# Kernel optimization log

Measured on AMD Instinct MI355X. Metric: run time of the kernel, lower is better.

The kernel has to match this reference:

```python
import jax, jax.numpy as jnp
import numpy as np

NUM_HEADS = 16
INACTIVE = 4          # cfg_comp.attention_heads_inactive
SIG_DIM = 64          # cfg_comp.attention_heads_signature_dim
MLP_HIDDEN = 512      # cfg_comp.attention_heads_inference_mlp_hidden


def setup_inputs() -> dict:
    key = jax.random.key(0)
    ks = jax.random.split(key, 16)
    S, B, E = 2048, 2, 1024
    def xavier(k, shape, gain=1.0):
        fan_in, fan_out = shape[1], shape[0]
        a = gain * np.sqrt(6.0 / (fan_in + fan_out))
        return jax.random.uniform(k, shape, jnp.float32, -a, a)
    g = 1.0 / np.sqrt(2.0)
    return {
        "query": jax.random.normal(ks[0], (S, B, E), jnp.float32),
        "q_w": xavier(ks[1], (E, E), g), "q_b": jnp.zeros((E,), jnp.float32),
        "k_w": xavier(ks[2], (E, E), g), "k_b": jnp.zeros((E,), jnp.float32),
        "v_w": xavier(ks[3], (E, E), g), "v_b": jnp.zeros((E,), jnp.float32),
        "out_w": xavier(ks[4], (E, E)), "out_b": jnp.zeros((E,), jnp.float32),
        "inf1_w": xavier(ks[5], (MLP_HIDDEN, E), np.sqrt(2.0)),
        "inf1_b": jnp.zeros((MLP_HIDDEN,), jnp.float32),
        "inf2_w": xavier(ks[6], (SIG_DIM, MLP_HIDDEN), np.sqrt(2.0)),
        "inf2_b": jnp.zeros((SIG_DIM,), jnp.float32),
        "head_sig": jax.random.normal(ks[7], (NUM_HEADS, SIG_DIM), jnp.float32)
                    * np.sqrt(2.0 / (NUM_HEADS + SIG_DIM)),
    }


def _head_mask(query, inf1_w, inf1_b, inf2_w, inf2_b, head_sig):
    # inference_masking_step: (S, B, E) -> binary mask (B, H, S)
    t = jax.nn.relu(query @ inf1_w.T + inf1_b)          # (S, B, hidden)
    t = t @ inf2_w.T + inf2_b                            # (S, B, sig)
    s = t @ head_sig.T                                   # (S, B, H) head scores
    keep = NUM_HEADS - INACTIVE
    kth = jax.lax.top_k(s, keep)[0][..., -1]             # (S, B) kth-largest score
    mask = (s >= kth[..., None]).astype(query.dtype)     # 1 at top-`keep` heads
    mask = jax.lax.stop_gradient(mask)                   # scatter of constants in torch
    return jnp.transpose(mask, (1, 2, 0))                # (B, H, S)


def reference(query, q_w, q_b, k_w, k_b, v_w, v_b, out_w, out_b,
              inf1_w, inf1_b, inf2_w, inf2_b, head_sig):
    S, B, E = query.shape
    H, D = NUM_HEADS, E // NUM_HEADS
    scaling = D ** (-0.5)

    q = (query @ q_w.T + q_b) * scaling                  # (S, B, E)
    k = query @ k_w.T + k_b
    v = query @ v_w.T + v_b
    # (S, B, E) -> (B, H, S, D)
    to_bhsd = lambda x: jnp.transpose(x.reshape(S, B, H, D), (1, 2, 0, 3))
    q, k, v = to_bhsd(q), to_bhsd(k), to_bhsd(v)

    attn = jax.nn.softmax(jnp.einsum("bhqd,bhkd->bhqk", q, k), axis=-1)
    o = jnp.einsum("bhqk,bhkd->bhqd", attn, v)           # (B, H, S, D)

    mask = _head_mask(query, inf1_w, inf1_b, inf2_w, inf2_b, head_sig)  # (B, H, S)
    o = o * mask[..., None]                              # gate per head per position

    out = jnp.transpose(o, (2, 0, 1, 3)).reshape(S, B, E)
    return out @ out_w.T + out_b
```

## Files before the change

kernel.cpp:

```cpp
#include <hip/hip_runtime.h>
#include <hip/hip_bf16.h>

#define S_LEN 2048
#define BATCH 2
#define EDIM 1024
#define NHEAD 16
#define DHEAD 64
#define HIDDEN 512
#define SIGD 64
#define KEEP 12

typedef __attribute__((ext_vector_type(8))) short bf16x8;
typedef __attribute__((ext_vector_type(4))) float f32x4;

static __device__ __forceinline__ float bf2f(short s) {
  unsigned int u = ((unsigned int)(unsigned short)s) << 16;
  float f; __builtin_memcpy(&f, &u, 4); return f;
}
static __device__ __forceinline__ short f2bf(float f) {
  unsigned int u; __builtin_memcpy(&u, &f, 4);
  u += 0x7fffu + ((u >> 16) & 1u);
  return (short)(u >> 16);
}

#if __has_builtin(__builtin_amdgcn_exp2f)
static __device__ __forceinline__ float fexp2(float x) { return __builtin_amdgcn_exp2f(x); }
#else
static __device__ __forceinline__ float fexp2(float x) { return exp2f(x); }
#endif

static __device__ __forceinline__ void gl_lds16(const short* g, short* l) {
  __builtin_amdgcn_global_load_lds(
      (const __attribute__((address_space(1))) unsigned int*)g,
      (__attribute__((address_space(3))) unsigned int*)l, 16, 0, 0);
}

template<int CTRL>
static __device__ __forceinline__ float dpp_movf(float x) {
  return __builtin_bit_cast(float, __builtin_amdgcn_update_dpp(
      0, __builtin_bit_cast(int, x), CTRL, 0xF, 0xF, true));
}
static __device__ __forceinline__ float row_max16(float v) {
  v = fmaxf(v, dpp_movf<0x128>(v));
  v = fmaxf(v, dpp_movf<0x124>(v));
  v = fmaxf(v, dpp_movf<0x122>(v));
  v = fmaxf(v, dpp_movf<0x121>(v));
  return v;
}
static __device__ __forceinline__ float row_sum16(float v) {
  v += dpp_movf<0x128>(v);
  v += dpp_movf<0x124>(v);
  v += dpp_movf<0x122>(v);
  v += dpp_movf<0x121>(v);
  return v;
}

__global__ __launch_bounds__(256) void cvt_all(
    const float* __restrict__ query, const float* __restrict__ inf1_w,
    const float* __restrict__ qw, const float* __restrict__ kw,
    const float* __restrict__ vw, const float* __restrict__ ow,
    short* __restrict__ qh, short* __restrict__ ql,
    short* __restrict__ w1h, short* __restrict__ w1l,
    short* __restrict__ Wq, short* __restrict__ Wk,
    short* __restrict__ Wv, short* __restrict__ Wo)
{
  int blk = blockIdx.x;
  if (blk < 4608) {
    const float* in; short *oh, *ol; int i;
    if (blk < 4096) { in = query;  oh = qh;  ol = ql;  i = (blk * 256 + threadIdx.x) * 4; }
    else            { in = inf1_w; oh = w1h; ol = w1l; i = ((blk - 4096) * 256 + threadIdx.x) * 4; }
    float4 f = *(const float4*)(in + i);
    union { short s[4]; uint2 v; } uh, ul;
    float x[4] = {f.x, f.y, f.z, f.w};
    #pragma unroll
    for (int u = 0; u < 4; ++u) {
      short h = f2bf(x[u]);
      uh.s[u] = h;
      ul.s[u] = f2bf(x[u] - bf2f(h));
    }
    *(uint2*)(oh + i) = uh.v;
    *(uint2*)(ol + i) = ul.v;
  } else {
    int t = blk - 4608;
    int mat = t >> 10, sub = t & 1023;
    const float* in = (mat == 0) ? qw : (mat == 1) ? kw : (mat == 2) ? vw : ow;
    short* out      = (mat == 0) ? Wq : (mat == 1) ? Wk : (mat == 2) ? Wv : Wo;
    int i = (sub * 256 + threadIdx.x) * 4;
    float4 f = *(const float4*)(in + i);
    union { short s[4]; uint2 v; } u;
    u.s[0] = f2bf(f.x); u.s[1] = f2bf(f.y); u.s[2] = f2bf(f.z); u.s[3] = f2bf(f.w);
    *(uint2*)(out + i) = u.v;
  }
}

template<bool F32OUT>
static __device__ __forceinline__ void gemm128_body(
    short* smem,
    const short* __restrict__ A, const short* __restrict__ B,
    const float* __restrict__ bias, void* __restrict__ outv,
    int row0, int col0, float scale)
{
  short* As = smem;
  short* Bs = smem + 128*32;
  const int tid  = threadIdx.x;
  const int wave = tid >> 6, lane = tid & 63;
  const int quad = lane >> 4, l16 = lane & 15;
  const int wr = wave >> 1, wc = wave & 1;
  const int lr = lane >> 2, lc8 = (lane & 3) * 8;

  const short* gA = A + (size_t)(row0 + wave*16 + lr) * EDIM + lc8;
  const short* gB = B + (size_t)(col0 + wave*16 + lr) * EDIM + lc8;
  short* lA = As + wave*512;
  short* lB = Bs + wave*512;

  f32x4 acc[4][4] = {};
  gl_lds16(gA, lA);  gl_lds16(gA + 64*EDIM, lA + 64*32);
  gl_lds16(gB, lB);  gl_lds16(gB + 64*EDIM, lB + 64*32);

  for (int k0 = 0; k0 < EDIM; k0 += 32) {
    __syncthreads();
    bf16x8 af[4], bfr[4];
    #pragma unroll
    for (int i = 0; i < 4; ++i)
      af[i] = *(const bf16x8*)&As[(wr*64 + i*16 + l16)*32 + quad*8];
    #pragma unroll
    for (int j = 0; j < 4; ++j)
      bfr[j] = *(const bf16x8*)&Bs[(wc*64 + j*16 + l16)*32 + quad*8];
    __syncthreads();
    if (k0 + 32 < EDIM) {
      const short* gA2 = gA + k0 + 32;
      const short* gB2 = gB + k0 + 32;
      gl_lds16(gA2, lA);  gl_lds16(gA2 + 64*EDIM, lA + 64*32);
      gl_lds16(gB2, lB);  gl_lds16(gB2 + 64*EDIM, lB + 64*32);
    }
    #pragma unroll
    for (int i = 0; i < 4; ++i)
      #pragma unroll
      for (int j = 0; j < 4; ++j)
        acc[i][j] = __builtin_amdgcn_mfma_f32_16x16x32_bf16(af[i], bfr[j], acc[i][j], 0, 0, 0);
  }
  #pragma unroll
  for (int j = 0; j < 4; ++j) {
    int col = col0 + wc*64 + j*16 + l16;
    float bv = bias[col];
    #pragma unroll
    for (int i = 0; i < 4; ++i) {
      int rowb = row0 + wr*64 + i*16 + quad*4;
      #pragma unroll
      for (int r = 0; r < 4; ++r) {
        float v = (acc[i][j][r] + bv) * scale;
        if constexpr (F32OUT) {
          ((float*)outv)[(size_t)(rowb + r) * EDIM + col] = v;
        } else {
          ((short*)outv)[(size_t)(rowb + r) * EDIM + col] = f2bf(v);
        }
      }
    }
  }
}

static __device__ __forceinline__ void gemm_t1_body(
    short* smem,
    const short* __restrict__ Agh, const short* __restrict__ Agl,
    const short* __restrict__ Bgh, const short* __restrict__ Bgl,
    const float* __restrict__ bias, float* __restrict__ T1,
    int row0, int col0)
{
  short* Ah = smem;
  short* Al = smem + 4096;
  short* Bh = smem + 8192;
  short* Bl = smem + 10240;
  const int tid  = threadIdx.x;
  const int wave = tid >> 6, lane = tid & 63;
  const int quad = lane >> 4, l16 = lane & 15;
  const int wr = wave >> 1, wc = wave & 1;
  const int lr = lane >> 2, lc8 = (lane & 3) * 8;

  const short* gAh = Agh + (size_t)(row0 + wave*16 + lr) * EDIM + lc8;
  const short* gAl = Agl + (size_t)(row0 + wave*16 + lr) * EDIM + lc8;
  const short* gBh = Bgh + (size_t)(col0 + wave*16 + lr) * EDIM + lc8;
  const short* gBl = Bgl + (size_t)(col0 + wave*16 + lr) * EDIM + lc8;
  short* lAh = Ah + wave*512;  short* lAl = Al + wave*512;
  short* lBh = Bh + wave*512;  short* lBl = Bl + wave*512;

  f32x4 acc[4][2] = {};
  gl_lds16(gAh, lAh);  gl_lds16(gAh + 64*EDIM, lAh + 64*32);
  gl_lds16(gAl, lAl);  gl_lds16(gAl + 64*EDIM, lAl + 64*32);
  gl_lds16(gBh, lBh);  gl_lds16(gBl, lBl);

  for (int k0 = 0; k0 < EDIM; k0 += 32) {
    __syncthreads();
    bf16x8 ah[4], al[4], bh[2], bl[2];
    #pragma unroll
    for (int i = 0; i < 4; ++i) {
      ah[i] = *(const bf16x8*)&Ah[(wr*64 + i*16 + l16)*32 + quad*8];
      al[i] = *(const bf16x8*)&Al[(wr*64 + i*16 + l16)*32 + quad*8];
    }
    #pragma unroll
    for (int j = 0; j < 2; ++j) {
      bh[j] = *(const bf16x8*)&Bh[(wc*32 + j*16 + l16)*32 + quad*8];
      bl[j] = *(const bf16x8*)&Bl[(wc*32 + j*16 + l16)*32 + quad*8];
    }
    __syncthreads();
    if (k0 + 32 < EDIM) {
      const short* p;
      p = gAh + k0 + 32;  gl_lds16(p, lAh);  gl_lds16(p + 64*EDIM, lAh + 64*32);
      p = gAl + k0 + 32;  gl_lds16(p, lAl);  gl_lds16(p + 64*EDIM, lAl + 64*32);
      gl_lds16(gBh + k0 + 32, lBh);  gl_lds16(gBl + k0 + 32, lBl);
    }
    #pragma unroll
    for (int i = 0; i < 4; ++i)
      #pragma unroll
      for (int j = 0; j < 2; ++j) {
        acc[i][j] = __builtin_amdgcn_mfma_f32_16x16x32_bf16(ah[i], bh[j], acc[i][j], 0, 0, 0);
        acc[i][j] = __builtin_amdgcn_mfma_f32_16x16x32_bf16(ah[i], bl[j], acc[i][j], 0, 0, 0);
        acc[i][j] = __builtin_amdgcn_mfma_f32_16x16x32_bf16(al[i], bh[j], acc[i][j], 0, 0, 0);
      }
  }
  #pragma unroll
  for (int j = 0; j < 2; ++j) {
    int col = col0 + wc*32 + j*16 + l16;
    float bv = bias[col];
    #pragma unroll
    for (int i = 0; i < 4; ++i) {
      int rowb = row0 + wr*64 + i*16 + quad*4;
      #pragma unroll
      for (int r = 0; r < 4; ++r)
        T1[(size_t)(rowb + r) * HIDDEN + col] = fmaxf(acc[i][j][r] + bv, 0.0f);
    }
  }
}

__global__ __launch_bounds__(256) void mega_gemm1(
    const short* __restrict__ qh, const short* __restrict__ ql,
    const short* __restrict__ w1h, const short* __restrict__ w1l,
    const float* __restrict__ inf1_b, float* __restrict__ T1,
    const short* __restrict__ Wq, const short* __restrict__ Wk,
    const short* __restrict__ Wv,
    const float* __restrict__ qb, const float* __restrict__ kb,
    const float* __restrict__ vb,
    short* __restrict__ Qp, short* __restrict__ Kp, short* __restrict__ Vp)
{
  __shared__ __attribute__((aligned(16))) short smem[12288];
  int blk = blockIdx.x;
  if ((blk & 3) == 3) {
    int id = blk >> 2;
    gemm_t1_body(smem, qh, ql, w1h, w1l, inf1_b, T1,
                 (id & 31) * 128, (id >> 5) * 64);
  } else {
    int id = (blk >> 2) * 3 + (blk & 3);
    int row0 = (id & 31) * 128;
    int rest = id >> 5;
    int mat = rest >> 3, cb = rest & 7;
    const short* B   = (mat == 0) ? Wq : (mat == 1) ? Wk : Wv;
    const float* bia = (mat == 0) ? qb : (mat == 1) ? kb : vb;
    short* out       = (mat == 0) ? Qp : (mat == 1) ? Kp : Vp;
    float scale      = (mat == 0) ? 0.18033688011112042f : 1.0f;
    gemm128_body<false>(smem, qh, B, bia, (void*)out, row0, cb * 128, scale);
  }
}

__global__ __launch_bounds__(256) void mid_kernel(
    const float* __restrict__ T1, const float* __restrict__ inf2_w,
    const float* __restrict__ inf2_b, const float* __restrict__ head_sig,
    float* __restrict__ maskbuf,
    const short* __restrict__ Vp, short* __restrict__ VT)
{
  __shared__ __attribute__((aligned(16))) float fsm[16*HIDDEN + 16*SIGD + 16*NHEAD];
  int blk = blockIdx.x;
  const int tid = threadIdx.x;
  if (blk < 256) {
    float (*t1s)[HIDDEN] = (float(*)[HIDDEN])fsm;
    float (*t2s)[SIGD]   = (float(*)[SIGD])(fsm + 16*HIDDEN);
    float (*ss)[NHEAD]   = (float(*)[NHEAD])(fsm + 16*HIDDEN + 16*SIGD);
    const int tok0 = blk * 16;
    {
      int row = tid >> 4, c0 = (tid & 15) * 32;
      const float* src = T1 + (size_t)(tok0 + row) * HIDDEN + c0;
      #pragma unroll
      for (int u = 0; u < 8; ++u)
        *(float4*)&t1s[row][c0 + u*4] = *(const float4*)(src + u*4);
    }
    __syncthreads();
    #pragma unroll
    for (int it = 0; it < 4; ++it) {
      int idx = tid + it * 256;
      int tok = idx >> 6, j = idx & 63;
      const float4* w4 = (const float4*)(inf2_w + (size_t)j * HIDDEN);
      const float4* t4 = (const float4*)(&t1s[tok][0]);
      float a = inf2_b[j];
      for (int k = 0; k < HIDDEN/4; ++k) {
        float4 wv = w4[k], tv = t4[k];
        a += tv.x*wv.x + tv.y*wv.y + tv.z*wv.z + tv.w*wv.w;
      }
      t2s[tok][j] = a;
    }
    __syncthreads();
    {
      int tok = tid >> 4, h = tid & 15;
      float a = 0.f;
      for (int d = 0; d < SIGD; ++d) a += t2s[tok][d] * head_sig[h*SIGD + d];
      ss[tok][h] = a;
    }
    __syncthreads();
    {
      int tok = tid >> 4, h = tid & 15;
      float sv = ss[tok][h];
      int cnt = 0;
      #pragma unroll
      for (int j = 0; j < NHEAD; ++j) cnt += (ss[tok][j] > sv) ? 1 : 0;
      int gt = tok0 + tok;
      int s = gt >> 1, b = gt & 1;
      maskbuf[((size_t)(b*NHEAD + h)) * S_LEN + s] = (cnt < KEEP) ? 1.0f : 0.0f;
    }
  } else {
    short (*tile)[72] = (short(*)[72])fsm;
    int t = blk - 256;
    const int s0 = (t & 31) * 64, e0 = ((t >> 5) & 15) * 64, b = t >> 9;
    {
      int sr = tid >> 2, ec = (tid & 3) * 16;
      const short* src = Vp + (size_t)(s0 + sr) * 2048 + b * 1024 + e0 + ec;
      *(uint4*)&tile[sr][ec]     = *(const uint4*)src;
      *(uint4*)&tile[sr][ec + 8] = *(const uint4*)(src + 8);
    }
    __syncthreads();
    {
      int er = tid >> 2, sc = (tid & 3) * 16;
      unsigned pack[8];
      #pragma unroll
      for (int u = 0; u < 8; ++u) {
        unsigned lo = (unsigned short)tile[sc + 2*u][er];
        unsigned hi = (unsigned short)tile[sc + 2*u + 1][er];
        pack[u] = lo | (hi << 16);
      }
      short* dst = VT + (size_t)(b * 1024 + e0 + er) * 2048 + s0 + sc;
      *(uint4*)(dst)     = *(uint4*)&pack[0];
      *(uint4*)(dst + 8) = *(uint4*)&pack[4];
    }
  }
}

__global__ __launch_bounds__(256) void flash_attn(
    short* QpOg, const short* __restrict__ Kp, const short* __restrict__ VT,
    const float* __restrict__ maskbuf)
{
  __shared__ __attribute__((aligned(16))) short Ks[128][72];
  __shared__ __attribute__((aligned(16))) short Vt[64*136];
  __shared__ __attribute__((aligned(16))) short uni[8704];
  const int bh = blockIdx.x;
  const int b = bh >> 4, h = bh & 15;
  const int q0 = blockIdx.y * 64;
  const int tid = threadIdx.x;
  const int wave = tid >> 6, lane = tid & 63;
  const int quad = lane >> 4, l16 = lane & 15;
  const size_t colbase = (size_t)b * EDIM + h * DHEAD;
  const size_t rstride = (size_t)BATCH * EDIM;
  const short* VTbase = VT + (size_t)(bh * 64) * S_LEN;
  {
    int r = tid >> 2, d0 = (tid & 3) * 16;
    const short* src = QpOg + (size_t)(q0 + r) * rstride + colbase + d0;
    *(uint4*)&uni[r*72 + d0]     = *(const uint4*)src;
    *(uint4*)&uni[r*72 + d0 + 8] = *(const uint4*)(src + 8);
  }
  __syncthreads();
  bf16x8 aq0 = *(const bf16x8*)&uni[(wave*16 + l16)*72 + quad*8];
  bf16x8 aq1 = *(const bf16x8*)&uni[(wave*16 + l16)*72 + 32 + quad*8];
  short* Psw = &uni[wave * 2176];

  float m_i[4], l_i[4];
  f32x4 oacc[4];
  #pragma unroll
  for (int r = 0; r < 4; ++r) { m_i[r] = -1e30f; l_i[r] = 0.f; }
  #pragma unroll
  for (int dt = 0; dt < 4; ++dt) oacc[dt] = f32x4{0.f, 0.f, 0.f, 0.f};

  const int vd  = tid >> 2;
  const int vcc = (((tid & 3) + vd) & 3) * 32;

  for (int kv0 = 0; kv0 < S_LEN; kv0 += 128) {
    __syncthreads();
    {
      int r = tid >> 1, c0 = (tid & 1) * 32;
      const short* src = Kp + (size_t)(kv0 + r) * rstride + colbase + c0;
      short* dst = &Ks[r][c0];
      *(uint4*)(dst)      = *(const uint4*)(src);
      *(uint4*)(dst + 8)  = *(const uint4*)(src + 8);
      *(uint4*)(dst + 16) = *(const uint4*)(src + 16);
      *(uint4*)(dst + 24) = *(const uint4*)(src + 24);
    }
    {
      const short* src = VTbase + (size_t)vd * S_LEN + kv0 + vcc;
      short* dst = &Vt[vd*136 + vcc];
      *(uint4*)(dst)      = *(const uint4*)(src);
      *(uint4*)(dst + 8)  = *(const uint4*)(src + 8);
      *(uint4*)(dst + 16) = *(const uint4*)(src + 16);
      *(uint4*)(dst + 24) = *(const uint4*)(src + 24);
    }
    __syncthreads();
    f32x4 sacc[8];
    #pragma unroll
    for (int c = 0; c < 8; ++c) sacc[c] = f32x4{0.f, 0.f, 0.f, 0.f};
    #pragma unroll
    for (int c = 0; c < 8; ++c) {
      bf16x8 b0 = *(const bf16x8*)&Ks[c*16 + l16][quad*8];
      bf16x8 b1 = *(const bf16x8*)&Ks[c*16 + l16][32 + quad*8];
      sacc[c] = __builtin_amdgcn_mfma_f32_16x16x32_bf16(aq0, b0, sacc[c], 0, 0, 0);
      sacc[c] = __builtin_amdgcn_mfma_f32_16x16x32_bf16(aq1, b1, sacc[c], 0, 0, 0);
    }
    #pragma unroll
    for (int r = 0; r < 4; ++r) {
      float vmax = sacc[0][r];
      #pragma unroll
      for (int c = 1; c < 8; ++c) vmax = fmaxf(vmax, sacc[c][r]);
      vmax = row_max16(vmax);
      float mnew = fmaxf(m_i[r], vmax);
      float alpha = fexp2(m_i[r] - mnew);
      float rsum = 0.f;
      short* prow = &Psw[(quad*4 + r)*136 + l16];
      #pragma unroll
      for (int p = 0; p < 4; ++p) {
        float ea = fexp2(sacc[2*p][r]   - mnew);
        float eb = fexp2(sacc[2*p+1][r] - mnew);
        unsigned pk = __builtin_amdgcn_perm(
            __builtin_bit_cast(unsigned, eb),
            __builtin_bit_cast(unsigned, ea), 0x07060302u);
        prow[(2*p)*16]     = (short)(pk & 0xffffu);
        prow[(2*p + 1)*16] = (short)(pk >> 16);
        rsum += ea + eb;
      }
      rsum = row_sum16(rsum);
      l_i[r] = l_i[r] * alpha + rsum;
      m_i[r] = mnew;
      #pragma unroll
      for (int dt = 0; dt < 4; ++dt) oacc[dt][r] *= alpha;
    }
    asm volatile("s_waitcnt lgkmcnt(0)" ::: "memory");
    #pragma unroll
    for (int ks = 0; ks < 4; ++ks) {
      bf16x8 ap = *(const bf16x8*)&Psw[l16*136 + ks*32 + quad*8];
      #pragma unroll
      for (int dt = 0; dt < 4; ++dt) {
        bf16x8 bb = *(const bf16x8*)&Vt[(dt*16 + l16)*136 + ks*32 + quad*8];
        oacc[dt] = __builtin_amdgcn_mfma_f32_16x16x32_bf16(ap, bb, oacc[dt], 0, 0, 0);
      }
    }
  }
  #pragma unroll
  for (int r = 0; r < 4; ++r) {
    int s = q0 + wave*16 + quad*4 + r;
    float mk = maskbuf[((size_t)(b*NHEAD + h)) * S_LEN + s];
    float scale = mk / l_i[r];
    short* dst = QpOg + (size_t)s * rstride + colbase;
    #pragma unroll
    for (int dt = 0; dt < 4; ++dt)
      dst[dt*16 + l16] = f2bf(oacc[dt][r] * scale);
  }
}

__global__ __launch_bounds__(256) void gemm_out(
    const short* __restrict__ A, const short* __restrict__ W,
    const float* __restrict__ bias, float* __restrict__ out)
{
  __shared__ __attribute__((aligned(16))) short smem[8192];
  gemm128_body<true>(smem, A, W, bias, (void*)out,
                     blockIdx.x * 128, blockIdx.y * 128, 1.0f);
}

extern "C" void kernel_launch(void* const* d_in, const int* in_sizes, int n_in,
                              void* d_out, int out_size, void* d_ws, size_t ws_size,
                              hipStream_t stream)
{
  const float* query   = (const float*)d_in[0];
  const float* q_w     = (const float*)d_in[1];
  const float* q_b     = (const float*)d_in[2];
  const float* k_w     = (const float*)d_in[3];
  const float* k_b     = (const float*)d_in[4];
  const float* v_w     = (const float*)d_in[5];
  const float* v_b     = (const float*)d_in[6];
  const float* out_w   = (const float*)d_in[7];
  const float* out_b   = (const float*)d_in[8];
  const float* inf1_w  = (const float*)d_in[9];
  const float* inf1_b  = (const float*)d_in[10];
  const float* inf2_w  = (const float*)d_in[11];
  const float* inf2_b  = (const float*)d_in[12];
  const float* head_sig= (const float*)d_in[13];

  char* ws = (char*)d_ws;
  short* qh      = (short*)(ws);
  short* VTb     = (short*)(ws);
  short* ql      = (short*)(ws + (size_t)( 8u<<20));
  float* maskbuf = (float*)(ws + (size_t)( 8u<<20));
  short* Qp      = (short*)(ws + (size_t)(16u<<20));
  short* Kp      = (short*)(ws + (size_t)(24u<<20));
  short* Vp      = (short*)(ws + (size_t)(32u<<20));
  short* Wo      = (short*)(ws + (size_t)(40u<<20));
  char* ob = (char*)d_out;
  float* T1  = (float*)(ob);
  short* w1h = (short*)(ob + (size_t)( 8u<<20));
  short* w1l = (short*)(ob + (size_t)( 9u<<20));
  short* Wq  = (short*)(ob + (size_t)(10u<<20));
  short* Wk  = (short*)(ob + (size_t)(12u<<20));
  short* Wv  = (short*)(ob + (size_t)(14u<<20));
  float* out = (float*)d_out;

  dim3 blk(256);
  cvt_all<<<dim3(8704), blk, 0, stream>>>(query, inf1_w, q_w, k_w, v_w, out_w,
                                          qh, ql, w1h, w1l, Wq, Wk, Wv, Wo);
  mega_gemm1<<<dim3(1024), blk, 0, stream>>>(qh, ql, w1h, w1l, inf1_b, T1,
                                             Wq, Wk, Wv, q_b, k_b, v_b, Qp, Kp, Vp);
  mid_kernel<<<dim3(1280), blk, 0, stream>>>(T1, inf2_w, inf2_b, head_sig, maskbuf,
                                             Vp, VTb);
  flash_attn<<<dim3(32, 32), blk, 0, stream>>>(Qp, Kp, VTb, maskbuf);
  gemm_out<<<dim3(32, 8), blk, 0, stream>>>(Qp, Wo, out_b, out);
}
```

Before: 338.8 us.

## Halve flash-attention KV tile and prefetch next tile into registers

The flash attention kernel now walks K/V in 64-row tiles instead of 128 and issues the global loads for the next tile into registers before computing on the current one. This hides global-load latency behind the MFMA and softmax work. The smaller tile also cuts LDS use, which can raise occupancy. MFMA sections are wrapped in s_setprio. The cost is twice as many loop iterations, each with two barriers and an online-softmax rescale.

```diff
diff --git a/kernel.cpp b/kernel.cpp
--- a/kernel.cpp
+++ b/kernel.cpp
@@ -344,9 +344,9 @@
     short* QpOg, const short* __restrict__ Kp, const short* __restrict__ VT,
     const float* __restrict__ maskbuf)
 {
-  __shared__ __attribute__((aligned(16))) short Ks[128][72];
-  __shared__ __attribute__((aligned(16))) short Vt[64*136];
-  __shared__ __attribute__((aligned(16))) short uni[8704];
+  __shared__ __attribute__((aligned(16))) short Ks[64][68];
+  __shared__ __attribute__((aligned(16))) short Vt[64][68];
+  __shared__ __attribute__((aligned(16))) short uni[4352];
   const int bh = blockIdx.x;
   const int b = bh >> 4, h = bh & 15;
   const int q0 = blockIdx.y * 64;
@@ -355,17 +355,23 @@
   const int quad = lane >> 4, l16 = lane & 15;
   const size_t colbase = (size_t)b * EDIM + h * DHEAD;
   const size_t rstride = (size_t)BATCH * EDIM;
-  const short* VTbase = VT + (size_t)(bh * 64) * S_LEN;
+
+  const int r4 = tid >> 2, c16 = (tid & 3) * 16;
+  const short* gK = Kp + (size_t)r4 * rstride + colbase + c16;
+  const short* gV = VT + (size_t)(bh * 64 + r4) * S_LEN + c16;
+
   {
-    int r = tid >> 2, d0 = (tid & 3) * 16;
-    const short* src = QpOg + (size_t)(q0 + r) * rstride + colbase + d0;
-    *(uint4*)&uni[r*72 + d0]     = *(const uint4*)src;
-    *(uint4*)&uni[r*72 + d0 + 8] = *(const uint4*)(src + 8);
+    const short* src = QpOg + (size_t)(q0 + r4) * rstride + colbase + c16;
+    *(uint4*)&uni[r4*68 + c16]     = *(const uint4*)src;
+    *(uint4*)&uni[r4*68 + c16 + 8] = *(const uint4*)(src + 8);
   }
   __syncthreads();
-  bf16x8 aq0 = *(const bf16x8*)&uni[(wave*16 + l16)*72 + quad*8];
-  bf16x8 aq1 = *(const bf16x8*)&uni[(wave*16 + l16)*72 + 32 + quad*8];
-  short* Psw = &uni[wave * 2176];
+  bf16x8 aq0 = *(const bf16x8*)&uni[(wave*16 + l16)*68 + quad*8];
+  bf16x8 aq1 = *(const bf16x8*)&uni[(wave*16 + l16)*68 + 32 + quad*8];
+  short* Psw = &uni[wave * 1088];
+
+  uint4 kr0 = *(const uint4*)(gK);      uint4 kr1 = *(const uint4*)(gK + 8);
+  uint4 vr0 = *(const uint4*)(gV);      uint4 vr1 = *(const uint4*)(gV + 8);
 
   float m_i[4], l_i[4];
   f32x4 oacc[4];
@@ -374,51 +380,42 @@
   #pragma unroll
   for (int dt = 0; dt < 4; ++dt) oacc[dt] = f32x4{0.f, 0.f, 0.f, 0.f};
 
-  const int vd  = tid >> 2;
-  const int vcc = (((tid & 3) + vd) & 3) * 32;
-
-  for (int kv0 = 0; kv0 < S_LEN; kv0 += 128) {
-    __syncthreads();
-    {
-      int r = tid >> 1, c0 = (tid & 1) * 32;
-      const short* src = Kp + (size_t)(kv0 + r) * rstride + colbase + c0;
-      short* dst = &Ks[r][c0];
-      *(uint4*)(dst)      = *(const uint4*)(src);
-      *(uint4*)(dst + 8)  = *(const uint4*)(src + 8);
-      *(uint4*)(dst + 16) = *(const uint4*)(src + 16);
-      *(uint4*)(dst + 24) = *(const uint4*)(src + 24);
-    }
-    {
-      const short* src = VTbase + (size_t)vd * S_LEN + kv0 + vcc;
-      short* dst = &Vt[vd*136 + vcc];
-      *(uint4*)(dst)      = *(const uint4*)(src);
-      *(uint4*)(dst + 8)  = *(const uint4*)(src + 8);
-      *(uint4*)(dst + 16) = *(const uint4*)(src + 16);
-      *(uint4*)(dst + 24) = *(const uint4*)(src + 24);
-    }
-    __syncthreads();
-    f32x4 sacc[8];
-    #pragma unroll
-    for (int c = 0; c < 8; ++c) sacc[c] = f32x4{0.f, 0.f, 0.f, 0.f};
-    #pragma unroll
-    for (int c = 0; c < 8; ++c) {
+  for (int kv0 = 0; kv0 < S_LEN; kv0 += 64) {
+    __syncthreads();
+    *(uint4*)&Ks[r4][c16]     = kr0;
+    *(uint4*)&Ks[r4][c16 + 8] = kr1;
+    *(uint4*)&Vt[r4][c16]     = vr0;
+    *(uint4*)&Vt[r4][c16 + 8] = vr1;
+    __syncthreads();
+    if (kv0 + 64 < S_LEN) {
+      const short* nK = gK + (size_t)(kv0 + 64) * rstride;
+      const short* nV = gV + (kv0 + 64);
+      kr0 = *(const uint4*)nK;  kr1 = *(const uint4*)(nK + 8);
+      vr0 = *(const uint4*)nV;  vr1 = *(const uint4*)(nV + 8);
+    }
+    f32x4 sacc[4];
+    #pragma unroll
+    for (int c = 0; c < 4; ++c) sacc[c] = f32x4{0.f, 0.f, 0.f, 0.f};
+    __builtin_amdgcn_s_setprio(1);
+    #pragma unroll
+    for (int c = 0; c < 4; ++c) {
       bf16x8 b0 = *(const bf16x8*)&Ks[c*16 + l16][quad*8];
       bf16x8 b1 = *(const bf16x8*)&Ks[c*16 + l16][32 + quad*8];
       sacc[c] = __builtin_amdgcn_mfma_f32_16x16x32_bf16(aq0, b0, sacc[c], 0, 0, 0);
       sacc[c] = __builtin_amdgcn_mfma_f32_16x16x32_bf16(aq1, b1, sacc[c], 0, 0, 0);
     }
+    __builtin_amdgcn_s_setprio(0);
     #pragma unroll
     for (int r = 0; r < 4; ++r) {
-      float vmax = sacc[0][r];
-      #pragma unroll
-      for (int c = 1; c < 8; ++c) vmax = fmaxf(vmax, sacc[c][r]);
+      float vmax = fmaxf(fmaxf(sacc[0][r], sacc[1][r]),
+                         fmaxf(sacc[2][r], sacc[3][r]));
       vmax = row_max16(vmax);
       float mnew = fmaxf(m_i[r], vmax);
       float alpha = fexp2(m_i[r] - mnew);
       float rsum = 0.f;
-      short* prow = &Psw[(quad*4 + r)*136 + l16];
-      #pragma unroll
-      for (int p = 0; p < 4; ++p) {
+      short* prow = &Psw[(quad*4 + r)*68 + l16];
+      #pragma unroll
+      for (int p = 0; p < 2; ++p) {
         float ea = fexp2(sacc[2*p][r]   - mnew);
         float eb = fexp2(sacc[2*p+1][r] - mnew);
         unsigned pk = __builtin_amdgcn_perm(
@@ -435,15 +432,17 @@
       for (int dt = 0; dt < 4; ++dt) oacc[dt][r] *= alpha;
     }
     asm volatile("s_waitcnt lgkmcnt(0)" ::: "memory");
-    #pragma unroll
-    for (int ks = 0; ks < 4; ++ks) {
-      bf16x8 ap = *(const bf16x8*)&Psw[l16*136 + ks*32 + quad*8];
+    __builtin_amdgcn_s_setprio(1);
+    #pragma unroll
+    for (int ks = 0; ks < 2; ++ks) {
+      bf16x8 ap = *(const bf16x8*)&Psw[l16*68 + ks*32 + quad*8];
       #pragma unroll
       for (int dt = 0; dt < 4; ++dt) {
-        bf16x8 bb = *(const bf16x8*)&Vt[(dt*16 + l16)*136 + ks*32 + quad*8];
+        bf16x8 bb = *(const bf16x8*)&Vt[dt*16 + l16][ks*32 + quad*8];
         oacc[dt] = __builtin_amdgcn_mfma_f32_16x16x32_bf16(ap, bb, oacc[dt], 0, 0, 0);
       }
     }
+    __builtin_amdgcn_s_setprio(0);
   }
   #pragma unroll
   for (int r = 0; r < 4; ++r) {
```

After: 353.8 us. 1.04x slower.

## Double query rows per flash-attention block with XOR-swizzled LDS and direct global-to-LDS loads

Applied to the files above, without the earlier changes.

The flash attention block now handles 128 query rows, each wave owning 32 rows as two 16-row halves. Every K and V fragment read from LDS therefore feeds twice as many MFMAs, and the grid is halved. K and V tiles are loaded with a global-to-LDS helper (gl_lds16) into XOR-swizzled unpadded layouts, replacing padded arrays and register-staged copies, and the P buffer is swizzled the same way. The cost is more accumulator registers per thread, 64KB of LDS per block, and fewer blocks (512), which may lower occupancy.

```diff
diff --git a/kernel.cpp b/kernel.cpp
--- a/kernel.cpp
+++ b/kernel.cpp
@@ -344,116 +344,153 @@
     short* QpOg, const short* __restrict__ Kp, const short* __restrict__ VT,
     const float* __restrict__ maskbuf)
 {
-  __shared__ __attribute__((aligned(16))) short Ks[128][72];
-  __shared__ __attribute__((aligned(16))) short Vt[64*136];
-  __shared__ __attribute__((aligned(16))) short uni[8704];
+  __shared__ __attribute__((aligned(16))) short smem[32768];
+  short* KsL = smem;
+  short* VtL = smem + 8192;
+  short* PsB = smem + 16384;
+  short* Qs  = smem + 16384;
+
   const int bh = blockIdx.x;
   const int b = bh >> 4, h = bh & 15;
-  const int q0 = blockIdx.y * 64;
+  const int q0 = blockIdx.y * 128;
   const int tid = threadIdx.x;
   const int wave = tid >> 6, lane = tid & 63;
   const int quad = lane >> 4, l16 = lane & 15;
   const size_t colbase = (size_t)b * EDIM + h * DHEAD;
   const size_t rstride = (size_t)BATCH * EDIM;
-  const short* VTbase = VT + (size_t)(bh * 64) * S_LEN;
+  short* Psw = PsB + wave * 4096;
+
   {
-    int r = tid >> 2, d0 = (tid & 3) * 16;
-    const short* src = QpOg + (size_t)(q0 + r) * rstride + colbase + d0;
-    *(uint4*)&uni[r*72 + d0]     = *(const uint4*)src;
-    *(uint4*)&uni[r*72 + d0 + 8] = *(const uint4*)(src + 8);
+    int row = tid >> 1;
+    int cb  = (tid & 1) * 4;
+    const short* src = QpOg + (size_t)(q0 + row) * rstride + colbase + cb * 8;
+    #pragma unroll
+    for (int u = 0; u < 4; ++u) {
+      uint4 v = *(const uint4*)(src + u * 8);
+      *(uint4*)&Qs[row * 64 + (((cb + u) ^ (row & 7)) * 8)] = v;
+    }
   }
   __syncthreads();
-  bf16x8 aq0 = *(const bf16x8*)&uni[(wave*16 + l16)*72 + quad*8];
-  bf16x8 aq1 = *(const bf16x8*)&uni[(wave*16 + l16)*72 + 32 + quad*8];
-  short* Psw = &uni[wave * 2176];
-
-  float m_i[4], l_i[4];
-  f32x4 oacc[4];
+  bf16x8 aq[2][2];
   #pragma unroll
-  for (int r = 0; r < 4; ++r) { m_i[r] = -1e30f; l_i[r] = 0.f; }
+  for (int h2 = 0; h2 < 2; ++h2)
+    #pragma unroll
+    for (int dh = 0; dh < 2; ++dh) {
+      int row = wave * 32 + h2 * 16 + l16;
+      aq[h2][dh] = *(const bf16x8*)&Qs[row * 64 + (((dh * 4 + quad) ^ (l16 & 7)) * 8)];
+    }
+
+  const int kxor = (lane & 7) ^ (lane >> 3);
+  const short* gKbase = Kp + colbase + (size_t)(wave * 32 + (lane >> 3)) * rstride + kxor * 8;
+  short* ldsK = KsL + wave * 2048;
+  const int vrow_l = lane >> 4;
+  short* ldsV = VtL + wave * 2048;
+
+  float m_i[2][4], l_i[2][4];
+  f32x4 oacc[2][4];
   #pragma unroll
-  for (int dt = 0; dt < 4; ++dt) oacc[dt] = f32x4{0.f, 0.f, 0.f, 0.f};
-
-  const int vd  = tid >> 2;
-  const int vcc = (((tid & 3) + vd) & 3) * 32;
+  for (int h2 = 0; h2 < 2; ++h2)
+    #pragma unroll
+    for (int r = 0; r < 4; ++r) { m_i[h2][r] = -1e30f; l_i[h2][r] = 0.f; }
+  #pragma unroll
+  for (int h2 = 0; h2 < 2; ++h2)
+    #pragma unroll
+    for (int dt = 0; dt < 4; ++dt) oacc[h2][dt] = f32x4{0.f, 0.f, 0.f, 0.f};
 
   for (int kv0 = 0; kv0 < S_LEN; kv0 += 128) {
     __syncthreads();
-    {
-      int r = tid >> 1, c0 = (tid & 1) * 32;
-      const short* src = Kp + (size_t)(kv0 + r) * rstride + colbase + c0;
-      short* dst = &Ks[r][c0];
-      *(uint4*)(dst)      = *(const uint4*)(src);
-      *(uint4*)(dst + 8)  = *(const uint4*)(src + 8);
-      *(uint4*)(dst + 16) = *(const uint4*)(src + 16);
-      *(uint4*)(dst + 24) = *(const uint4*)(src + 24);
-    }
-    {
-      const short* src = VTbase + (size_t)vd * S_LEN + kv0 + vcc;
-      short* dst = &Vt[vd*136 + vcc];
-      *(uint4*)(dst)      = *(const uint4*)(src);
-      *(uint4*)(dst + 8)  = *(const uint4*)(src + 8);
-      *(uint4*)(dst + 16) = *(const uint4*)(src + 16);
-      *(uint4*)(dst + 24) = *(const uint4*)(src + 24);
-    }
-    __syncthreads();
-    f32x4 sacc[8];
-    #pragma unroll
-    for (int c = 0; c < 8; ++c) sacc[c] = f32x4{0.f, 0.f, 0.f, 0.f};
+    #pragma unroll
+    for (int i = 0; i < 4; ++i) {
+      gl_lds16(gKbase + (size_t)(kv0 + i * 8) * rstride, ldsK + i * 512);
+      int vrow = wave * 16 + i * 4 + vrow_l;
+      int vx = (lane & 15) ^ ((i & 1) * 4 + vrow_l);
+      gl_lds16(VT + (size_t)(bh * 64 + vrow) * S_LEN + kv0 + vx * 8, ldsV + i * 512);
+    }
+    asm volatile("s_waitcnt vmcnt(0)" ::: "memory");
+    __syncthreads();
+
+    f32x4 sacc[2][8];
+    #pragma unroll
+    for (int h2 = 0; h2 < 2; ++h2)
+      #pragma unroll
+      for (int c = 0; c < 8; ++c) sacc[h2][c] = f32x4{0.f, 0.f, 0.f, 0.f};
     #pragma unroll
     for (int c = 0; c < 8; ++c) {
-      bf16x8 b0 = *(const bf16x8*)&Ks[c*16 + l16][quad*8];
-      bf16x8 b1 = *(const bf16x8*)&Ks[c*16 + l16][32 + quad*8];
-      sacc[c] = __builtin_amdgcn_mfma_f32_16x16x32_bf16(aq0, b0, sacc[c], 0, 0, 0);
-      sacc[c] = __builtin_amdgcn_mfma_f32_16x16x32_bf16(aq1, b1, sacc[c], 0, 0, 0);
-    }
+      const short* kr = &KsL[(c * 16 + l16) * 64];
+      bf16x8 b0 = *(const bf16x8*)&kr[((quad     ^ (l16 & 7)) * 8)];
+      bf16x8 b1 = *(const bf16x8*)&kr[(((4 + quad) ^ (l16 & 7)) * 8)];
+      #pragma unroll
+      for (int h2 = 0; h2 < 2; ++h2) {
+        sacc[h2][c] = __builtin_amdgcn_mfma_f32_16x16x32_bf16(aq[h2][0], b0, sacc[h2][c], 0, 0, 0);
+        sacc[h2][c] = __builtin_amdgcn_mfma_f32_16x16x32_bf16(aq[h2][1], b1, sacc[h2][c], 0, 0, 0);
+      }
+    }
+
+    #pragma unroll
+    for (int h2 = 0; h2 < 2; ++h2) {
+      #pragma unroll
+      for (int r = 0; r < 4; ++r) {
+        float vmax = fmaxf(fmaxf(fmaxf(sacc[h2][0][r], sacc[h2][1][r]),
+                                 fmaxf(sacc[h2][2][r], sacc[h2][3][r])),
+                           fmaxf(fmaxf(sacc[h2][4][r], sacc[h2][5][r]),
+                                 fmaxf(sacc[h2][6][r], sacc[h2][7][r])));
+        vmax = row_max16(vmax);
+        float mnew = fmaxf(m_i[h2][r], vmax);
+        float alpha = fexp2(m_i[h2][r] - mnew);
+        float rsum = 0.f;
+        int row = h2 * 16 + quad * 4 + r;
+        int sw = quad * 2 + (r >> 1);
+        #pragma unroll
+        for (int p = 0; p < 4; ++p) {
+          float ea = fexp2(sacc[h2][2*p][r]   - mnew);
+          float eb = fexp2(sacc[h2][2*p+1][r] - mnew);
+          unsigned pk = __builtin_amdgcn_perm(
+              __builtin_bit_cast(unsigned, eb),
+              __builtin_bit_cast(unsigned, ea), 0x07060302u);
+          short* pb = Psw + (p >> 1) * 2048 + row * 64;
+          int c1 = ((2*p) & 3) * 2 + (l16 >> 3);
+          int c2 = ((2*p+1) & 3) * 2 + (l16 >> 3);
+          pb[((c1 ^ sw) * 8) + (l16 & 7)] = (short)(pk & 0xffffu);
+          pb[((c2 ^ sw) * 8) + (l16 & 7)] = (short)(pk >> 16);
+          rsum += ea + eb;
+        }
+        rsum = row_sum16(rsum);
+        l_i[h2][r] = l_i[h2][r] * alpha + rsum;
+        m_i[h2][r] = mnew;
+        #pragma unroll
+        for (int dt = 0; dt < 4; ++dt) oacc[h2][dt][r] *= alpha;
+      }
+    }
+    asm volatile("s_waitcnt lgkmcnt(0)" ::: "memory");
+
+    #pragma unroll
+    for (int ks = 0; ks < 4; ++ks) {
+      const short* p0 = Psw + (ks >> 1) * 2048;
+      int pc = (((ks & 1) * 4 + quad) ^ (l16 >> 1)) * 8;
+      bf16x8 ap0 = *(const bf16x8*)&p0[l16 * 64 + pc];
+      bf16x8 ap1 = *(const bf16x8*)&p0[(16 + l16) * 64 + pc];
+      #pragma unroll
+      for (int dt = 0; dt < 4; ++dt) {
+        bf16x8 bb = *(const bf16x8*)&VtL[(dt * 16 + l16) * 128 +
+                                         (((ks * 4 + quad) ^ (l16 & 7)) * 8)];
+        oacc[0][dt] = __builtin_amdgcn_mfma_f32_16x16x32_bf16(ap0, bb, oacc[0][dt], 0, 0, 0);
+        oacc[1][dt] = __builtin_amdgcn_mfma_f32_16x16x32_bf16(ap1, bb, oacc[1][dt], 0, 0, 0);
+      }
+    }
+  }
+
+  #pragma unroll
+  for (int h2 = 0; h2 < 2; ++h2) {
     #pragma unroll
     for (int r = 0; r < 4; ++r) {
-      float vmax = sacc[0][r];
-      #pragma unroll
-      for (int c = 1; c < 8; ++c) vmax = fmaxf(vmax, sacc[c][r]);
-      vmax = row_max16(vmax);
-      float mnew = fmaxf(m_i[r], vmax);
-      float alpha = fexp2(m_i[r] - mnew);
-      float rsum = 0.f;
-      short* prow = &Psw[(quad*4 + r)*136 + l16];
-      #pragma unroll
-      for (int p = 0; p < 4; ++p) {
-        float ea = fexp2(sacc[2*p][r]   - mnew);
-        float eb = fexp2(sacc[2*p+1][r] - mnew);
-        unsigned pk = __builtin_amdgcn_perm(
-            __builtin_bit_cast(unsigned, eb),
-            __builtin_bit_cast(unsigned, ea), 0x07060302u);
-        prow[(2*p)*16]     = (short)(pk & 0xffffu);
-        prow[(2*p + 1)*16] = (short)(pk >> 16);
-        rsum += ea + eb;
-      }
-      rsum = row_sum16(rsum);
-      l_i[r] = l_i[r] * alpha + rsum;
-      m_i[r] = mnew;
-      #pragma unroll
-      for (int dt = 0; dt < 4; ++dt) oacc[dt][r] *= alpha;
-    }
-    asm volatile("s_waitcnt lgkmcnt(0)" ::: "memory");
-    #pragma unroll
-    for (int ks = 0; ks < 4; ++ks) {
-      bf16x8 ap = *(const bf16x8*)&Psw[l16*136 + ks*32 + quad*8];
-      #pragma unroll
-      for (int dt = 0; dt < 4; ++dt) {
-        bf16x8 bb = *(const bf16x8*)&Vt[(dt*16 + l16)*136 + ks*32 + quad*8];
-        oacc[dt] = __builtin_amdgcn_mfma_f32_16x16x32_bf16(ap, bb, oacc[dt], 0, 0, 0);
-      }
-    }
-  }
-  #pragma unroll
-  for (int r = 0; r < 4; ++r) {
-    int s = q0 + wave*16 + quad*4 + r;
-    float mk = maskbuf[((size_t)(b*NHEAD + h)) * S_LEN + s];
-    float scale = mk / l_i[r];
-    short* dst = QpOg + (size_t)s * rstride + colbase;
-    #pragma unroll
-    for (int dt = 0; dt < 4; ++dt)
-      dst[dt*16 + l16] = f2bf(oacc[dt][r] * scale);
+      int s = q0 + wave * 32 + h2 * 16 + quad * 4 + r;
+      float mk = maskbuf[((size_t)(b * NHEAD + h)) * S_LEN + s];
+      float scale = mk / l_i[h2][r];
+      short* dst = QpOg + (size_t)s * rstride + colbase;
+      #pragma unroll
+      for (int dt = 0; dt < 4; ++dt)
+        dst[dt * 16 + l16] = f2bf(oacc[h2][dt][r] * scale);
+    }
   }
 }
 
@@ -510,6 +547,6 @@
                                              Wq, Wk, Wv, q_b, k_b, v_b, Qp, Kp, Vp);
   mid_kernel<<<dim3(1280), blk, 0, stream>>>(T1, inf2_w, inf2_b, head_sig, maskbuf,
                                              Vp, VTb);
-  flash_attn<<<dim3(32, 32), blk, 0, stream>>>(Qp, Kp, VTb, maskbuf);
+  flash_attn<<<dim3(32, 16), blk, 0, stream>>>(Qp, Kp, VTb, maskbuf);
   gemm_out<<<dim3(32, 8), blk, 0, stream>>>(Qp, Wo, out_b, out);
 }
```

Result: faster. 320.8 us (-5.3%).
